# Performance work log

Measured on AMD Instinct MI355X. Metric: run time of the kernel, lower is better.

## Reference

```python
import jax, jax.numpy as jnp
import numpy as np
from jax import lax

NUM_TAGS = 64

def setup_inputs() -> dict:
    key = jax.random.key(0)
    ks = jax.random.split(key, 6)
    B, T, D, N = 64, 512, 1024, NUM_TAGS
    inputs = jax.random.normal(ks[0], (B, T, D), dtype=jnp.float32)
    mask = jnp.ones((B, T), dtype=jnp.int32)
    labels = jax.random.randint(ks[1], (B, T), 0, N)
    W = jax.random.normal(ks[2], (D, N), dtype=jnp.float32) / np.sqrt(D).astype(np.float32)
    b = jnp.zeros((N,), dtype=jnp.float32)
    transitions = jax.random.normal(ks[3], (N, N), dtype=jnp.float32) * 0.1
    start_transitions = jax.random.normal(ks[4], (N,), dtype=jnp.float32) * 0.1
    end_transitions = jax.random.normal(ks[5], (N,), dtype=jnp.float32) * 0.1
    return dict(inputs=inputs, mask=mask, labels=labels, W=W, b=b,
                transitions=transitions, start_transitions=start_transitions,
                end_transitions=end_transitions)


def _log_partition(logits, mask, trans, start, end):
    # forward algorithm (log-sum-exp recurrence). logits [B,T,N], mask bool [B,T]
    alpha = start[None, :] + logits[:, 0]                      # [B,N]
    emits = jnp.swapaxes(logits, 0, 1)[1:]                     # [T-1,B,N]
    ms = jnp.swapaxes(mask, 0, 1)[1:, :, None]                 # [T-1,B,1]
    def step(alpha, xs):
        emit, m = xs
        inner = alpha[:, :, None] + trans[None] + emit[:, None, :]  # [B,from,to]
        new = jax.nn.logsumexp(inner, axis=1)
        return jnp.where(m, new, alpha), None
    alpha, _ = lax.scan(step, alpha, (emits, ms))
    return jax.nn.logsumexp(alpha + end[None, :], axis=-1)     # [B]


def _joint_score(logits, tags, mask, trans, start, end):
    # score of the gold tag sequence (AllenNLP _joint_likelihood), vectorized
    maskf = mask.astype(logits.dtype)
    score = start[tags[:, 0]]
    score = score + jnp.sum(trans[tags[:, :-1], tags[:, 1:]] * maskf[:, 1:], axis=1)
    emit = jnp.take_along_axis(logits, tags[:, :, None], axis=2)[:, :, 0]   # [B,T]
    score = score + jnp.sum(emit * maskf, axis=1)
    last_idx = jnp.sum(mask.astype(jnp.int32), axis=1) - 1
    last_tags = jnp.take_along_axis(tags, last_idx[:, None], axis=1)[:, 0]
    return score + end[last_tags]


def _viterbi(logits, mask, trans, start, end):
    # batched Viterbi decode with backpointers; masked steps carry state through
    B, T, N = logits.shape
    alpha = start[None, :] + logits[:, 0]
    emits = jnp.swapaxes(logits, 0, 1)[1:]
    ms = jnp.swapaxes(mask, 0, 1)[1:, :, None]
    ident = jnp.broadcast_to(jnp.arange(N, dtype=jnp.int32)[None, :], (B, N))
    def step(alpha, xs):
        emit, m = xs
        sc = alpha[:, :, None] + trans[None] + emit[:, None, :]  # [B,from,to]
        best = jnp.max(sc, axis=1)
        bp = jnp.argmax(sc, axis=1).astype(jnp.int32)
        return jnp.where(m, best, alpha), jnp.where(m, bp, ident)
    alpha, bps = lax.scan(step, alpha, (emits, ms))
    last_tag = jnp.argmax(alpha + end[None, :], axis=-1).astype(jnp.int32)
    def back(tag, bp):
        prev = jnp.take_along_axis(bp, tag[:, None], axis=1)[:, 0]
        return prev, tag
    first, rest = lax.scan(back, last_tag, bps, reverse=True)
    tags = jnp.concatenate([first[None], rest], axis=0)          # [T,B]
    return jnp.swapaxes(tags, 0, 1) * mask.astype(jnp.int32)     # zero out padding


def reference(inputs, mask, labels, W, b, transitions, start_transitions, end_transitions):
    bool_mask = mask.astype(bool)
    logits = inputs @ W + b                                      # tag projection [B,T,N]
    scores = logits * mask[..., None].astype(logits.dtype)       # scores = inputs * mask
    tags = _viterbi(scores, bool_mask, transitions, start_transitions, end_transitions)
    log_z = _log_partition(scores, bool_mask, transitions, start_transitions, end_transitions)
    gold = _joint_score(scores, labels, bool_mask, transitions, start_transitions, end_transitions)
    loss = jnp.mean(log_z - gold)                                # mean negative log-likelihood
    return scores, tags, loss
```

## Files before the change

### kernel.cpp

```cpp
#include <hip/hip_runtime.h>
#include <cstdint>
#include <cstddef>

#define BB 64
#define TT 512
#define DD 1024
#define NTAG 64
#define CUT 255
#define SCORES_ELEMS (BB * TT * NTAG)
#define TAGS_OFF SCORES_ELEMS
#define LOSS_OFF (SCORES_ELEMS + BB * TT)

typedef __attribute__((ext_vector_type(8))) short short8;
typedef __attribute__((ext_vector_type(4))) float floatx4;
typedef __attribute__((ext_vector_type(16))) float f32x16;

__device__ __forceinline__ unsigned short f2bf_rne(float x) {
  const unsigned int u = __float_as_uint(x);
  const unsigned int r = u + 0x7FFFu + ((u >> 16) & 1u);
  return (unsigned short)(r >> 16);
}
__device__ __forceinline__ float bf2f(unsigned short h) {
  return __uint_as_float(((unsigned int)h) << 16);
}

__device__ __forceinline__ void block_sync_lds() {
  asm volatile("s_waitcnt lgkmcnt(0)\n\ts_barrier" ::: "memory");
}

__device__ __forceinline__ float quad_xor1(float v) {
  int x = __builtin_amdgcn_update_dpp(__float_as_int(v), __float_as_int(v), 0xB1, 0xf, 0xf, false);
  return __int_as_float(x);
}
__device__ __forceinline__ float quad_xor2(float v) {
  int x = __builtin_amdgcn_update_dpp(__float_as_int(v), __float_as_int(v), 0x4E, 0xf, 0xf, false);
  return __int_as_float(x);
}

__device__ __forceinline__ float dpp_red_max(float v) {
  int x;
  x = __builtin_amdgcn_update_dpp(__float_as_int(v), __float_as_int(v), 0x111, 0xf, 0xf, false);
  v = fmaxf(v, __int_as_float(x));
  x = __builtin_amdgcn_update_dpp(__float_as_int(v), __float_as_int(v), 0x112, 0xf, 0xf, false);
  v = fmaxf(v, __int_as_float(x));
  x = __builtin_amdgcn_update_dpp(__float_as_int(v), __float_as_int(v), 0x114, 0xf, 0xf, false);
  v = fmaxf(v, __int_as_float(x));
  x = __builtin_amdgcn_update_dpp(__float_as_int(v), __float_as_int(v), 0x118, 0xf, 0xf, false);
  v = fmaxf(v, __int_as_float(x));
  x = __builtin_amdgcn_update_dpp(__float_as_int(v), __float_as_int(v), 0x142, 0xa, 0xf, false);
  v = fmaxf(v, __int_as_float(x));
  x = __builtin_amdgcn_update_dpp(__float_as_int(v), __float_as_int(v), 0x143, 0xc, 0xf, false);
  v = fmaxf(v, __int_as_float(x));
  return __int_as_float(__builtin_amdgcn_readlane(__float_as_int(v), 63));
}

__device__ __forceinline__ float dpp_red_sum(float v) {
  int x;
  x = __builtin_amdgcn_update_dpp(__float_as_int(v), __float_as_int(v), 0x111, 0xf, 0xf, false);
  v = v + __int_as_float(x);
  x = __builtin_amdgcn_update_dpp(__float_as_int(v), __float_as_int(v), 0x112, 0xf, 0xf, false);
  v = v + __int_as_float(x);
  x = __builtin_amdgcn_update_dpp(__float_as_int(v), __float_as_int(v), 0x114, 0xf, 0xf, false);
  v = v + __int_as_float(x);
  x = __builtin_amdgcn_update_dpp(__float_as_int(v), __float_as_int(v), 0x118, 0xf, 0xf, false);
  v = v + __int_as_float(x);
  x = __builtin_amdgcn_update_dpp(__float_as_int(v), __float_as_int(v), 0x142, 0xa, 0xf, false);
  v = v + __int_as_float(x);
  x = __builtin_amdgcn_update_dpp(__float_as_int(v), __float_as_int(v), 0x143, 0xc, 0xf, false);
  v = v + __int_as_float(x);
  return __int_as_float(__builtin_amdgcn_readlane(__float_as_int(v), 63));
}

__global__ __launch_bounds__(256) void prep_w(
    const float* __restrict__ W, unsigned short* __restrict__ wf_hi,
    unsigned short* __restrict__ wf_lo) {
  const int f = blockIdx.x * 256 + threadIdx.x;
  const int kk = f >> 8;
  const int nt = (f >> 6) & 3;
  const int l = f & 63;
  const int n = nt * 16 + (l & 15);
  const int k0 = kk * 32 + ((l >> 4) << 3);
  short8 hv, lv;
#pragma unroll
  for (int j = 0; j < 8; ++j) {
    const float x = W[(size_t)(k0 + j) * NTAG + n];
    const unsigned short h = f2bf_rne(x);
    hv[j] = (short)h;
    lv[j] = (short)f2bf_rne(x - bf2f(h));
  }
  *reinterpret_cast<short8*>(wf_hi + (size_t)f * 8) = hv;
  *reinterpret_cast<short8*>(wf_lo + (size_t)f * 8) = lv;
}

__global__ __launch_bounds__(256) void gemm_scores(
    const float* __restrict__ X, const int* __restrict__ mask,
    const unsigned short* __restrict__ wf_hi,
    const unsigned short* __restrict__ wf_lo,
    const float* __restrict__ bias, float* __restrict__ scores) {
  __shared__ unsigned short xhi[64 * 72];
  __shared__ unsigned short xlo[64 * 72];
  const int tid = threadIdx.x;
  const int lane = tid & 63;
  const int wv = tid >> 6;
  const int row0 = blockIdx.x * 64;
  const int srow = tid >> 2;
  const int scg = tid & 3;
  const float* Xp = X + (size_t)(row0 + srow) * DD + scg * 16;

  floatx4 acc[4];
#pragma unroll
  for (int nt = 0; nt < 4; ++nt) acc[nt] = (floatx4)(0.f);

  float4 px[4];
#pragma unroll
  for (int p = 0; p < 4; ++p) px[p] = *reinterpret_cast<const float4*>(Xp + p * 4);

  const int arow = (wv << 4) + (lane & 15);
  const int aq = (lane >> 4) << 3;

  for (int c = 0; c < 16; ++c) {
    __syncthreads();
    short8 hb0, hb1, lb0, lb1;
#pragma unroll
    for (int p = 0; p < 4; ++p) {
      const float v[4] = {px[p].x, px[p].y, px[p].z, px[p].w};
#pragma unroll
      for (int e = 0; e < 4; ++e) {
        const unsigned short h = f2bf_rne(v[e]);
        const unsigned short lo2 = f2bf_rne(v[e] - bf2f(h));
        const int idx = p * 4 + e;
        if (idx < 8) { hb0[idx] = (short)h; lb0[idx] = (short)lo2; }
        else         { hb1[idx - 8] = (short)h; lb1[idx - 8] = (short)lo2; }
      }
    }
    {
      const int base = srow * 72 + scg * 16;
      *reinterpret_cast<short8*>(&xhi[base]) = hb0;
      *reinterpret_cast<short8*>(&xhi[base + 8]) = hb1;
      *reinterpret_cast<short8*>(&xlo[base]) = lb0;
      *reinterpret_cast<short8*>(&xlo[base + 8]) = lb1;
    }
    const int cn = (c < 15) ? (c + 1) : 0;
#pragma unroll
    for (int p = 0; p < 4; ++p)
      px[p] = *reinterpret_cast<const float4*>(Xp + cn * 64 + p * 4);
    __syncthreads();

#pragma unroll
    for (int sub = 0; sub < 2; ++sub) {
      const int kkAbs = c * 2 + sub;
      const short8 ah = *reinterpret_cast<const short8*>(&xhi[arow * 72 + sub * 32 + aq]);
      const short8 al = *reinterpret_cast<const short8*>(&xlo[arow * 72 + sub * 32 + aq]);
      const size_t fbase = (size_t)kkAbs * 4 * 64 * 8;
#pragma unroll
      for (int nt = 0; nt < 4; ++nt) {
        const size_t off = fbase + ((size_t)nt * 64 + lane) * 8;
        const short8 bh = *reinterpret_cast<const short8*>(wf_hi + off);
        const short8 bl = *reinterpret_cast<const short8*>(wf_lo + off);
        acc[nt] = __builtin_amdgcn_mfma_f32_16x16x32_bf16(ah, bh, acc[nt], 0, 0, 0);
        acc[nt] = __builtin_amdgcn_mfma_f32_16x16x32_bf16(ah, bl, acc[nt], 0, 0, 0);
        acc[nt] = __builtin_amdgcn_mfma_f32_16x16x32_bf16(al, bh, acc[nt], 0, 0, 0);
      }
    }
  }

  const int colb = lane & 15;
  const int quad = lane >> 4;
#pragma unroll
  for (int r = 0; r < 4; ++r) {
    const int row = row0 + (wv << 4) + quad * 4 + r;
    const float mf = (float)mask[row];
#pragma unroll
    for (int nt = 0; nt < 4; ++nt) {
      const int col = nt * 16 + colb;
      scores[(size_t)row * 64 + col] = (acc[nt][r] + bias[col]) * mf;
    }
  }
}

__global__ __launch_bounds__(256, 1) void crf_forward(
    const float* __restrict__ scores, const int* __restrict__ mask,
    const float* __restrict__ trans, const float* __restrict__ startv,
    const float* __restrict__ endv, float* __restrict__ ws_alpha,
    float* __restrict__ ws_beta, float* __restrict__ zAcut,
    float* __restrict__ bScut, float* __restrict__ bVcut,
    float* __restrict__ Ca, float* __restrict__ Cb) {
  __shared__ float zbuf[2][NTAG];
  __shared__ float part[4];
  const int tid = threadIdx.x;
  const int wv = tid >> 6;
  const int lane = tid & 63;
  const int q = lane & 3;
  const int jl = lane >> 2;
  const int j = wv * 16 + jl;
  const int role = blockIdx.x >> 6;
  const int b = blockIdx.x & 63;
  const float* sc = scores + (size_t)b * TT * NTAG;
  const int* maskb = mask + b * TT;

  if (role == 0) {
    f32x16 tc;
#pragma unroll
    for (int i2 = 0; i2 < 16; ++i2)
      tc[i2] = trans[(size_t)(16 * q + i2) * NTAG + j];

    float aj = startv[j] + sc[j];
    if (q == 0) zbuf[0][j] = aj;
    float* wsA = ws_alpha + (size_t)b * 256 * NTAG;

    float e0 = sc[1 * NTAG + j], e1 = sc[2 * NTAG + j];
    float e2 = sc[3 * NTAG + j], e3 = sc[4 * NTAG + j];
    int k0 = maskb[1], k1 = maskb[2], k2 = maskb[3], k3 = maskb[4];
    __syncthreads();

    int cur = 0;
    for (int t = 1; t <= CUT; ++t) {
      if (q == 0) wsA[(size_t)(t - 1) * NTAG + j] = aj;
      const float4 a0 = *reinterpret_cast<const float4*>(&zbuf[cur][q * 16 + 0]);
      const float4 a1 = *reinterpret_cast<const float4*>(&zbuf[cur][q * 16 + 4]);
      const float4 a2 = *reinterpret_cast<const float4*>(&zbuf[cur][q * 16 + 8]);
      const float4 a3 = *reinterpret_cast<const float4*>(&zbuf[cur][q * 16 + 12]);
      const float emit = e0;
      const int m = k0;
      const int tp = (t + 4 <= CUT) ? (t + 4) : CUT;
      e0 = e1; e1 = e2; e2 = e3;
      e3 = sc[(size_t)tp * NTAG + j];
      k0 = k1; k1 = k2; k2 = k3;
      k3 = maskb[tp];

      const float c0 = a0.x + tc[0],  c1 = a0.y + tc[1];
      const float c2 = a0.z + tc[2],  c3 = a0.w + tc[3];
      const float c4 = a1.x + tc[4],  c5 = a1.y + tc[5];
      const float c6 = a1.z + tc[6],  c7 = a1.w + tc[7];
      const float c8 = a2.x + tc[8],  c9 = a2.y + tc[9];
      const float cA = a2.z + tc[10], cB = a2.w + tc[11];
      const float cC = a3.x + tc[12], cD = a3.y + tc[13];
      const float cE = a3.z + tc[14], cF = a3.w + tc[15];
      const float h0 = fmaxf(fmaxf(c0, c1), fmaxf(c2, c3));
      const float h1 = fmaxf(fmaxf(c4, c5), fmaxf(c6, c7));
      const float h2 = fmaxf(fmaxf(c8, c9), fmaxf(cA, cB));
      const float h3 = fmaxf(fmaxf(cC, cD), fmaxf(cE, cF));
      float pm = fmaxf(fmaxf(h0, h1), fmaxf(h2, h3));
      pm = fmaxf(pm, quad_xor1(pm));
      pm = fmaxf(pm, quad_xor2(pm));

      aj = m ? (pm + emit) : aj;
      const int nxt = cur ^ 1;
      if (q == 0) zbuf[nxt][j] = aj;
      block_sync_lds();
      cur = nxt;
    }
    if (q == 0) wsA[(size_t)255 * NTAG + j] = aj;
  } else if (role == 1) {
    f32x16 ec;
#pragma unroll
    for (int i2 = 0; i2 < 16; ++i2)
      ec[i2] = expf(trans[(size_t)(16 * q + i2) * NTAG + j]);

    const float a0v = startv[j] + sc[j];
    const float wm = dpp_red_max(a0v);
    if (lane == 0) part[wv] = wm;
    __syncthreads();
    const float M0 = fmaxf(fmaxf(part[0], part[1]), fmaxf(part[2], part[3]));
    float zj = expf(a0v - M0);
    float C = M0;
    if (q == 0) zbuf[0][j] = zj;

    float e0 = sc[1 * NTAG + j], e1 = sc[2 * NTAG + j];
    float e2 = sc[3 * NTAG + j], e3 = sc[4 * NTAG + j];
    int k0 = maskb[1], k1 = maskb[2], k2 = maskb[3], k3 = maskb[4];
    float pe = expf(e0);
    __syncthreads();

    int cur = 0;
    for (int t = 1; t <= CUT; ++t) {
      const float4 z0 = *reinterpret_cast<const float4*>(&zbuf[cur][q * 16 + 0]);
      const float4 z1 = *reinterpret_cast<const float4*>(&zbuf[cur][q * 16 + 4]);
      const float4 z2 = *reinterpret_cast<const float4*>(&zbuf[cur][q * 16 + 8]);
      const float4 z3 = *reinterpret_cast<const float4*>(&zbuf[cur][q * 16 + 12]);
      const float pec = pe;
      const int m = k0;
      const int tp = (t + 4 <= CUT) ? (t + 4) : CUT;
      e0 = e1; e1 = e2; e2 = e3;
      e3 = sc[(size_t)tp * NTAG + j];
      k0 = k1; k1 = k2; k2 = k3;
      k3 = maskb[tp];
      pe = expf(e0);

      float s0 = z0.x * ec[0], s1 = z0.y * ec[1];
      float s2 = z0.z * ec[2], s3 = z0.w * ec[3];
      s0 = fmaf(z1.x, ec[4], s0);  s1 = fmaf(z1.y, ec[5], s1);
      s2 = fmaf(z1.z, ec[6], s2);  s3 = fmaf(z1.w, ec[7], s3);
      s0 = fmaf(z2.x, ec[8], s0);  s1 = fmaf(z2.y, ec[9], s1);
      s2 = fmaf(z2.z, ec[10], s2); s3 = fmaf(z2.w, ec[11], s3);
      s0 = fmaf(z3.x, ec[12], s0); s1 = fmaf(z3.y, ec[13], s1);
      s2 = fmaf(z3.z, ec[14], s2); s3 = fmaf(z3.w, ec[15], s3);
      float s = (s0 + s1) + (s2 + s3);
      s += quad_xor1(s);
      s += quad_xor2(s);

      zj = m ? (s * pec) : zj;

      if ((t & 7) == 0) {
        const float ws = dpp_red_sum(zj);
        if (lane == 0) part[wv] = ws;
        block_sync_lds();
        const float S4 = (part[0] + part[1]) + (part[2] + part[3]);
        const float r = __builtin_amdgcn_rcpf(S4);
        zj *= 4.0f * r;
        C += logf(S4) - 1.3862943611198906f;
      }

      const int nxt = cur ^ 1;
      if (q == 0) zbuf[nxt][j] = zj;
      block_sync_lds();
      cur = nxt;
    }
    if (q == 0) zAcut[b * NTAG + j] = zj;
    if (tid == 0) Ca[b] = C;
  } else if (role == 2) {
    f32x16 tc;
#pragma unroll
    for (int i2 = 0; i2 < 16; ++i2)
      tc[i2] = trans[(size_t)j * NTAG + 16 * q + i2];

    float bj = endv[j];
    float* wsB = ws_beta + (size_t)b * 256 * NTAG;
    if (q == 0) {
      wsB[(size_t)255 * NTAG + j] = bj;
      zbuf[0][j] = bj + sc[(size_t)511 * NTAG + j];
    }
    float e0 = sc[(size_t)510 * NTAG + j], e1 = sc[(size_t)509 * NTAG + j];
    float e2 = sc[(size_t)508 * NTAG + j], e3 = sc[(size_t)507 * NTAG + j];
    int k0 = maskb[511], k1 = maskb[510], k2 = maskb[509], k3 = maskb[508];
    __syncthreads();

    int cur = 0;
    for (int t = 511; t >= 257; --t) {
      const float4 a0 = *reinterpret_cast<const float4*>(&zbuf[cur][q * 16 + 0]);
      const float4 a1 = *reinterpret_cast<const float4*>(&zbuf[cur][q * 16 + 4]);
      const float4 a2 = *reinterpret_cast<const float4*>(&zbuf[cur][q * 16 + 8]);
      const float4 a3 = *reinterpret_cast<const float4*>(&zbuf[cur][q * 16 + 12]);
      const float emit = e0;
      const int m = k0;
      const int tpe = (t - 5 >= 0) ? (t - 5) : 0;
      const int tpk = (t - 4 >= 256) ? (t - 4) : 256;
      e0 = e1; e1 = e2; e2 = e3;
      e3 = sc[(size_t)tpe * NTAG + j];
      k0 = k1; k1 = k2; k2 = k3;
      k3 = maskb[tpk];

      const float c0 = a0.x + tc[0],  c1 = a0.y + tc[1];
      const float c2 = a0.z + tc[2],  c3 = a0.w + tc[3];
      const float c4 = a1.x + tc[4],  c5 = a1.y + tc[5];
      const float c6 = a1.z + tc[6],  c7 = a1.w + tc[7];
      const float c8 = a2.x + tc[8],  c9 = a2.y + tc[9];
      const float cA = a2.z + tc[10], cB = a2.w + tc[11];
      const float cC = a3.x + tc[12], cD = a3.y + tc[13];
      const float cE = a3.z + tc[14], cF = a3.w + tc[15];
      const float h0 = fmaxf(fmaxf(c0, c1), fmaxf(c2, c3));
      const float h1 = fmaxf(fmaxf(c4, c5), fmaxf(c6, c7));
      const float h2 = fmaxf(fmaxf(c8, c9), fmaxf(cA, cB));
      const float h3 = fmaxf(fmaxf(cC, cD), fmaxf(cE, cF));
      float pm = fmaxf(fmaxf(h0, h1), fmaxf(h2, h3));
      pm = fmaxf(pm, quad_xor1(pm));
      pm = fmaxf(pm, quad_xor2(pm));

      bj = m ? pm : bj;
      const int nxt = cur ^ 1;
      if (q == 0) {
        wsB[(size_t)(t - 1 - 256) * NTAG + j] = bj;
        zbuf[nxt][j] = bj + emit;
      }
      block_sync_lds();
      cur = nxt;
    }
    {
      const float4 a0 = *reinterpret_cast<const float4*>(&zbuf[cur][q * 16 + 0]);
      const float4 a1 = *reinterpret_cast<const float4*>(&zbuf[cur][q * 16 + 4]);
      const float4 a2 = *reinterpret_cast<const float4*>(&zbuf[cur][q * 16 + 8]);
      const float4 a3 = *reinterpret_cast<const float4*>(&zbuf[cur][q * 16 + 12]);
      const float c0 = a0.x + tc[0],  c1 = a0.y + tc[1];
      const float c2 = a0.z + tc[2],  c3 = a0.w + tc[3];
      const float c4 = a1.x + tc[4],  c5 = a1.y + tc[5];
      const float c6 = a1.z + tc[6],  c7 = a1.w + tc[7];
      const float c8 = a2.x + tc[8],  c9 = a2.y + tc[9];
      const float cA = a2.z + tc[10], cB = a2.w + tc[11];
      const float cC = a3.x + tc[12], cD = a3.y + tc[13];
      const float cE = a3.z + tc[14], cF = a3.w + tc[15];
      const float h0 = fmaxf(fmaxf(c0, c1), fmaxf(c2, c3));
      const float h1 = fmaxf(fmaxf(c4, c5), fmaxf(c6, c7));
      const float h2 = fmaxf(fmaxf(c8, c9), fmaxf(cA, cB));
      const float h3 = fmaxf(fmaxf(cC, cD), fmaxf(cE, cF));
      float pm = fmaxf(fmaxf(h0, h1), fmaxf(h2, h3));
      pm = fmaxf(pm, quad_xor1(pm));
      pm = fmaxf(pm, quad_xor2(pm));
      bj = k0 ? pm : bj;
      if (q == 0) bVcut[b * NTAG + j] = bj;
    }
  } else {
    f32x16 ec;
#pragma unroll
    for (int i2 = 0; i2 < 16; ++i2)
      ec[i2] = expf(trans[(size_t)j * NTAG + 16 * q + i2]);

    float bj = expf(endv[j]);
    float C = 0.f;
    if (q == 0) zbuf[0][j] = bj * expf(sc[(size_t)511 * NTAG + j]);
    float e0 = sc[(size_t)510 * NTAG + j], e1 = sc[(size_t)509 * NTAG + j];
    float e2 = sc[(size_t)508 * NTAG + j], e3 = sc[(size_t)507 * NTAG + j];
    int k0 = maskb[511], k1 = maskb[510], k2 = maskb[509], k3 = maskb[508];
    float pe = expf(e0);
    __syncthreads();

    int cur = 0;
    for (int t = 511; t >= 257; --t) {
      const float4 z0 = *reinterpret_cast<const float4*>(&zbuf[cur][q * 16 + 0]);
      const float4 z1 = *reinterpret_cast<const float4*>(&zbuf[cur][q * 16 + 4]);
      const float4 z2 = *reinterpret_cast<const float4*>(&zbuf[cur][q * 16 + 8]);
      const float4 z3 = *reinterpret_cast<const float4*>(&zbuf[cur][q * 16 + 12]);
      const float pec = pe;
      const int m = k0;
      const int tpe = (t - 5 >= 0) ? (t - 5) : 0;
      const int tpk = (t - 4 >= 256) ? (t - 4) : 256;
      e0 = e1; e1 = e2; e2 = e3;
      e3 = sc[(size_t)tpe * NTAG + j];
      k0 = k1; k1 = k2; k2 = k3;
      k3 = maskb[tpk];
      pe = expf(e0);

      float s0 = z0.x * ec[0], s1 = z0.y * ec[1];
      float s2 = z0.z * ec[2], s3 = z0.w * ec[3];
      s0 = fmaf(z1.x, ec[4], s0);  s1 = fmaf(z1.y, ec[5], s1);
      s2 = fmaf(z1.z, ec[6], s2);  s3 = fmaf(z1.w, ec[7], s3);
      s0 = fmaf(z2.x, ec[8], s0);  s1 = fmaf(z2.y, ec[9], s1);
      s2 = fmaf(z2.z, ec[10], s2); s3 = fmaf(z2.w, ec[11], s3);
      s0 = fmaf(z3.x, ec[12], s0); s1 = fmaf(z3.y, ec[13], s1);
      s2 = fmaf(z3.z, ec[14], s2); s3 = fmaf(z3.w, ec[15], s3);
      float s = (s0 + s1) + (s2 + s3);
      s += quad_xor1(s);
      s += quad_xor2(s);

      bj = m ? s : bj;

      if ((t & 7) == 0) {
        const float ws = dpp_red_sum(bj);
        if (lane == 0) part[wv] = ws;
        block_sync_lds();
        const float S4 = (part[0] + part[1]) + (part[2] + part[3]);
        const float r = __builtin_amdgcn_rcpf(S4);
        bj *= 4.0f * r;
        C += logf(S4) - 1.3862943611198906f;
      }

      const int nxt = cur ^ 1;
      if (q == 0) zbuf[nxt][j] = bj * pec;
      block_sync_lds();
      cur = nxt;
    }
    {
      const float4 z0 = *reinterpret_cast<const float4*>(&zbuf[cur][q * 16 + 0]);
      const float4 z1 = *reinterpret_cast<const float4*>(&zbuf[cur][q * 16 + 4]);
      const float4 z2 = *reinterpret_cast<const float4*>(&zbuf[cur][q * 16 + 8]);
      const float4 z3 = *reinterpret_cast<const float4*>(&zbuf[cur][q * 16 + 12]);
      float s0 = z0.x * ec[0], s1 = z0.y * ec[1];
      float s2 = z0.z * ec[2], s3 = z0.w * ec[3];
      s0 = fmaf(z1.x, ec[4], s0);  s1 = fmaf(z1.y, ec[5], s1);
      s2 = fmaf(z1.z, ec[6], s2);  s3 = fmaf(z1.w, ec[7], s3);
      s0 = fmaf(z2.x, ec[8], s0);  s1 = fmaf(z2.y, ec[9], s1);
      s2 = fmaf(z2.z, ec[10], s2); s3 = fmaf(z2.w, ec[11], s3);
      s0 = fmaf(z3.x, ec[12], s0); s1 = fmaf(z3.y, ec[13], s1);
      s2 = fmaf(z3.z, ec[14], s2); s3 = fmaf(z3.w, ec[15], s3);
      float s = (s0 + s1) + (s2 + s3);
      s += quad_xor1(s);
      s += quad_xor2(s);
      bj = k0 ? s : bj;
      if (q == 0) bScut[b * NTAG + j] = bj;
      if (tid == 0) Cb[b] = C;
    }
  }
}

__global__ __launch_bounds__(64, 1) void crf_combine(
    const float* __restrict__ scores, const int* __restrict__ mask,
    const int* __restrict__ labels, const float* __restrict__ trans,
    const float* __restrict__ startv, const float* __restrict__ endv,
    const float* __restrict__ ws_alpha, const float* __restrict__ bVcut,
    const float* __restrict__ zAcut, const float* __restrict__ bScut,
    const float* __restrict__ Ca, const float* __restrict__ Cb,
    int* __restrict__ ws_lasttag, float* __restrict__ ws_loss) {
  const int lane = threadIdx.x;
  const int b = blockIdx.x;
  const float* sc = scores + (size_t)b * TT * NTAG;
  const int* maskb = mask + b * TT;

  const float aV = ws_alpha[((size_t)b * 256 + 255) * NTAG + lane];
  const float fv = aV + bVcut[b * NTAG + lane];
  const float mx = dpp_red_max(fv);
  const int jstar = (int)__builtin_ctzll(__ballot(fv == mx));
  if (lane == 0) ws_lasttag[b] = jstar;

  const float S = dpp_red_sum(zAcut[b * NTAG + lane] * bScut[b * NTAG + lane]);
  const float log_z = logf(S) + Ca[b] + Cb[b];

  float g = 0.f, msumf = 0.f;
  for (int t = lane; t < TT; t += 64) {
    const int lab = labels[b * TT + t];
    const float mf = (float)maskb[t];
    msumf += mf;
    g += sc[(size_t)t * NTAG + lab] * mf;
    if (t >= 1) {
      const int labp = labels[b * TT + t - 1];
      g += trans[(size_t)labp * NTAG + lab] * mf;
    }
  }
  g = dpp_red_sum(g);
  const float msum = dpp_red_sum(msumf);
  const int last_idx = (int)msum - 1;
  g += startv[labels[b * TT]] + endv[labels[b * TT + last_idx]];
  if (lane == 0) ws_loss[b] = log_z - g;
}

__global__ __launch_bounds__(64, 1) void viterbi_bt(
    const float* __restrict__ ws_alpha, const float* __restrict__ ws_beta,
    const int* __restrict__ ws_lasttag, const int* __restrict__ mask,
    const float* __restrict__ scores, const float* __restrict__ trans,
    float* __restrict__ out_tags) {
  __shared__ float tP[NTAG * 65];
  __shared__ int mk[256];
  __shared__ unsigned char tagb[256];
  const int lane = threadIdx.x;
  const int role = blockIdx.x >> 6;
  const int b = blockIdx.x & 63;

#pragma unroll
  for (int i = 0; i < NTAG; ++i) tP[i * 65 + lane] = trans[(size_t)i * NTAG + lane];
  const int tbase = role * 256;
  for (int t = lane; t < 256; t += 64) mk[t] = mask[b * TT + tbase + t];
  __syncthreads();

  int jcur = ws_lasttag[b];

  if (role == 0) {
    const float* wsA = ws_alpha + (size_t)b * 256 * NTAG;
    if (lane == 0) tagb[255] = (unsigned char)jcur;

    float a0 = wsA[(size_t)254 * NTAG + lane];
    float a1 = wsA[(size_t)253 * NTAG + lane];
    float a2 = wsA[(size_t)252 * NTAG + lane];
    float a3 = wsA[(size_t)251 * NTAG + lane];

    for (int s = 254; s >= 0; --s) {
      const float ac = a0;
      a0 = a1; a1 = a2; a2 = a3;
      const int sp = (s >= 4) ? (s - 4) : 0;
      a3 = wsA[(size_t)sp * NTAG + lane];
      if (mk[s + 1]) {
        const float c = ac + tP[lane * 65 + jcur];
        const float cmx = dpp_red_max(c);
        jcur = (int)__builtin_ctzll(__ballot(c == cmx));
      }
      if (lane == 0) tagb[s] = (unsigned char)jcur;
    }
  } else {
    const float* wsB = ws_beta + (size_t)b * 256 * NTAG;
    const float* scb = scores + (size_t)b * TT * NTAG;
    float r0 = wsB[(size_t)0 * NTAG + lane], r1 = wsB[(size_t)1 * NTAG + lane];
    float r2 = wsB[(size_t)2 * NTAG + lane], r3 = wsB[(size_t)3 * NTAG + lane];
    float s0 = scb[(size_t)256 * NTAG + lane], s1 = scb[(size_t)257 * NTAG + lane];
    float s2 = scb[(size_t)258 * NTAG + lane], s3 = scb[(size_t)259 * NTAG + lane];

    for (int t = 256; t < TT; ++t) {
      const float bv = r0, sv = s0;
      const int tb = (t + 4 < TT) ? (t + 4) : (TT - 1);
      r0 = r1; r1 = r2; r2 = r3;
      r3 = wsB[(size_t)(tb - 256) * NTAG + lane];
      s0 = s1; s1 = s2; s2 = s3;
      s3 = scb[(size_t)tb * NTAG + lane];
      if (mk[t - 256]) {
        const float c = tP[jcur * 65 + lane] + sv + bv;
        const float cmx = dpp_red_max(c);
        jcur = (int)__builtin_ctzll(__ballot(c == cmx));
      }
      if (lane == 0) tagb[t - 256] = (unsigned char)jcur;
    }
  }
  __syncthreads();
  for (int t = lane; t < 256; t += 64)
    out_tags[b * TT + tbase + t] = (float)(mk[t] ? (int)tagb[t] : 0);
}

__global__ __launch_bounds__(64, 1) void loss_mean(const float* __restrict__ ws_loss,
                                                   float* __restrict__ out) {
  const float v = ws_loss[threadIdx.x];
  const float s = dpp_red_sum(v);
  if (threadIdx.x == 0) out[0] = s * (1.0f / 64.0f);
}

extern "C" void kernel_launch(void* const* d_in, const int* in_sizes, int n_in,
                              void* d_out, int out_size, void* d_ws, size_t ws_size,
                              hipStream_t stream) {
  const float* X = (const float*)d_in[0];
  const int* mask = (const int*)d_in[1];
  const int* labels = (const int*)d_in[2];
  const float* W = (const float*)d_in[3];
  const float* bias = (const float*)d_in[4];
  const float* trans = (const float*)d_in[5];
  const float* startv = (const float*)d_in[6];
  const float* endv = (const float*)d_in[7];

  float* out = (float*)d_out;
  float* scores = out;
  float* out_tags = out + TAGS_OFF;
  float* out_loss = out + LOSS_OFF;

  unsigned short* wf_hi = (unsigned short*)d_ws;
  unsigned short* wf_lo = wf_hi + 65536;
  float* ws_alpha = (float*)(wf_lo + 65536);
  float* ws_beta = ws_alpha + (size_t)BB * 256 * NTAG;
  float* zAcut = ws_beta + (size_t)BB * 256 * NTAG;
  float* bScut = zAcut + BB * NTAG;
  float* bVcut = bScut + BB * NTAG;
  float* Ca = bVcut + BB * NTAG;
  float* Cb = Ca + BB;
  int* ws_lasttag = (int*)(Cb + BB);
  float* ws_loss = (float*)(ws_lasttag + BB);

  prep_w<<<32, 256, 0, stream>>>(W, wf_hi, wf_lo);
  gemm_scores<<<512, 256, 0, stream>>>(X, mask, wf_hi, wf_lo, bias, scores);
  crf_forward<<<256, 256, 0, stream>>>(scores, mask, trans, startv, endv,
                                       ws_alpha, ws_beta, zAcut, bScut, bVcut,
                                       Ca, Cb);
  crf_combine<<<64, 64, 0, stream>>>(scores, mask, labels, trans, startv, endv,
                                     ws_alpha, bVcut, zAcut, bScut, Ca, Cb,
                                     ws_lasttag, ws_loss);
  viterbi_bt<<<128, 64, 0, stream>>>(ws_alpha, ws_beta, ws_lasttag, mask,
                                     scores, trans, out_tags);
  loss_mean<<<1, 64, 0, stream>>>(ws_loss, out_loss);
}
```

Baseline: 394.0 us.

## Split GEMM K dimension across waves with LDS reduction, shrink row tile

The scores GEMM now gives each block 16 rows instead of 64 and splits the K=1024 reduction across the four waves, 256 each. Each wave loads its X fragment straight from global into registers, so the LDS staging and per-chunk barriers are gone. A single LDS reduction at the end combines the partial sums, and the grid grows to 2048 blocks with a higher occupancy hint. This is meant to expose more parallelism and memory-level concurrency for this memory-bound GEMM, at the cost of an extra reduction step and each block rereading all of W.

```diff
diff --git a/kernel.cpp b/kernel.cpp
--- a/kernel.cpp
+++ b/kernel.cpp
@@ -92,88 +92,84 @@
   *reinterpret_cast<short8*>(wf_lo + (size_t)f * 8) = lv;
 }
 
-__global__ __launch_bounds__(256) void gemm_scores(
+__global__ __launch_bounds__(256, 6) void gemm_scores(
     const float* __restrict__ X, const int* __restrict__ mask,
     const unsigned short* __restrict__ wf_hi,
     const unsigned short* __restrict__ wf_lo,
     const float* __restrict__ bias, float* __restrict__ scores) {
-  __shared__ unsigned short xhi[64 * 72];
-  __shared__ unsigned short xlo[64 * 72];
+  __shared__ float red[3 * 64 * 17];
   const int tid = threadIdx.x;
   const int lane = tid & 63;
   const int wv = tid >> 6;
-  const int row0 = blockIdx.x * 64;
-  const int srow = tid >> 2;
-  const int scg = tid & 3;
-  const float* Xp = X + (size_t)(row0 + srow) * DD + scg * 16;
+  const int row0 = blockIdx.x * 16;
+  const int arow = row0 + (lane & 15);
+  const int aq = (lane >> 4) << 3;
+  const float* Ap = X + (size_t)arow * DD + wv * 256 + aq;
 
   floatx4 acc[4];
 #pragma unroll
   for (int nt = 0; nt < 4; ++nt) acc[nt] = (floatx4)(0.f);
 
-  float4 px[4];
-#pragma unroll
-  for (int p = 0; p < 4; ++p) px[p] = *reinterpret_cast<const float4*>(Xp + p * 4);
-
-  const int arow = (wv << 4) + (lane & 15);
-  const int aq = (lane >> 4) << 3;
-
-  for (int c = 0; c < 16; ++c) {
-    __syncthreads();
-    short8 hb0, hb1, lb0, lb1;
-#pragma unroll
-    for (int p = 0; p < 4; ++p) {
-      const float v[4] = {px[p].x, px[p].y, px[p].z, px[p].w};
-#pragma unroll
-      for (int e = 0; e < 4; ++e) {
+  float4 a0 = *reinterpret_cast<const float4*>(Ap);
+  float4 a1 = *reinterpret_cast<const float4*>(Ap + 4);
+
+#pragma unroll
+  for (int kk = 0; kk < 8; ++kk) {
+    short8 ah, al;
+    {
+      const float v[8] = {a0.x, a0.y, a0.z, a0.w, a1.x, a1.y, a1.z, a1.w};
+#pragma unroll
+      for (int e = 0; e < 8; ++e) {
         const unsigned short h = f2bf_rne(v[e]);
-        const unsigned short lo2 = f2bf_rne(v[e] - bf2f(h));
-        const int idx = p * 4 + e;
-        if (idx < 8) { hb0[idx] = (short)h; lb0[idx] = (short)lo2; }
-        else         { hb1[idx - 8] = (short)h; lb1[idx - 8] = (short)lo2; }
+        ah[e] = (short)h;
+        al[e] = (short)f2bf_rne(v[e] - bf2f(h));
       }
     }
-    {
-      const int base = srow * 72 + scg * 16;
-      *reinterpret_cast<short8*>(&xhi[base]) = hb0;
-      *reinterpret_cast<short8*>(&xhi[base + 8]) = hb1;
-      *reinterpret_cast<short8*>(&xlo[base]) = lb0;
-      *reinterpret_cast<short8*>(&xlo[base + 8]) = lb1;
-    }
-    const int cn = (c < 15) ? (c + 1) : 0;
-#pragma unroll
-    for (int p = 0; p < 4; ++p)
-      px[p] = *reinterpret_cast<const float4*>(Xp + cn * 64 + p * 4);
-    __syncthreads();
-
-#pragma unroll
-    for (int sub = 0; sub < 2; ++sub) {
-      const int kkAbs = c * 2 + sub;
-      const short8 ah = *reinterpret_cast<const short8*>(&xhi[arow * 72 + sub * 32 + aq]);
-      const short8 al = *reinterpret_cast<const short8*>(&xlo[arow * 72 + sub * 32 + aq]);
-      const size_t fbase = (size_t)kkAbs * 4 * 64 * 8;
+    if (kk < 7) {
+      a0 = *reinterpret_cast<const float4*>(Ap + (kk + 1) * 32);
+      a1 = *reinterpret_cast<const float4*>(Ap + (kk + 1) * 32 + 4);
+    }
+    const int kkAbs = wv * 8 + kk;
+    const size_t fbase = (size_t)kkAbs * 4 * 64 * 8;
+#pragma unroll
+    for (int nt = 0; nt < 4; ++nt) {
+      const size_t off = fbase + ((size_t)nt * 64 + lane) * 8;
+      const short8 bh = *reinterpret_cast<const short8*>(wf_hi + off);
+      const short8 bl = *reinterpret_cast<const short8*>(wf_lo + off);
+      acc[nt] = __builtin_amdgcn_mfma_f32_16x16x32_bf16(ah, bh, acc[nt], 0, 0, 0);
+      acc[nt] = __builtin_amdgcn_mfma_f32_16x16x32_bf16(ah, bl, acc[nt], 0, 0, 0);
+      acc[nt] = __builtin_amdgcn_mfma_f32_16x16x32_bf16(al, bh, acc[nt], 0, 0, 0);
+    }
+  }
+
+  if (wv > 0) {
+    float* dst = &red[((wv - 1) * 64 + lane) * 17];
+#pragma unroll
+    for (int nt = 0; nt < 4; ++nt)
+#pragma unroll
+      for (int r = 0; r < 4; ++r) dst[nt * 4 + r] = acc[nt][r];
+  }
+  __syncthreads();
+  if (wv == 0) {
+#pragma unroll
+    for (int w = 0; w < 3; ++w) {
+      const float* srcp = &red[(w * 64 + lane) * 17];
+#pragma unroll
+      for (int nt = 0; nt < 4; ++nt)
+#pragma unroll
+        for (int r = 0; r < 4; ++r) acc[nt][r] += srcp[nt * 4 + r];
+    }
+    const int colb = lane & 15;
+    const int quad = lane >> 4;
+#pragma unroll
+    for (int r = 0; r < 4; ++r) {
+      const int row = row0 + quad * 4 + r;
+      const float mf = (float)mask[row];
 #pragma unroll
       for (int nt = 0; nt < 4; ++nt) {
-        const size_t off = fbase + ((size_t)nt * 64 + lane) * 8;
-        const short8 bh = *reinterpret_cast<const short8*>(wf_hi + off);
-        const short8 bl = *reinterpret_cast<const short8*>(wf_lo + off);
-        acc[nt] = __builtin_amdgcn_mfma_f32_16x16x32_bf16(ah, bh, acc[nt], 0, 0, 0);
-        acc[nt] = __builtin_amdgcn_mfma_f32_16x16x32_bf16(ah, bl, acc[nt], 0, 0, 0);
-        acc[nt] = __builtin_amdgcn_mfma_f32_16x16x32_bf16(al, bh, acc[nt], 0, 0, 0);
+        const int col = nt * 16 + colb;
+        scores[(size_t)row * 64 + col] = (acc[nt][r] + bias[col]) * mf;
       }
-    }
-  }
-
-  const int colb = lane & 15;
-  const int quad = lane >> 4;
-#pragma unroll
-  for (int r = 0; r < 4; ++r) {
-    const int row = row0 + (wv << 4) + quad * 4 + r;
-    const float mf = (float)mask[row];
-#pragma unroll
-    for (int nt = 0; nt < 4; ++nt) {
-      const int col = nt * 16 + colb;
-      scores[(size_t)row * 64 + col] = (acc[nt][r] + bias[col]) * mf;
     }
   }
 }
@@ -627,7 +623,7 @@
   float* ws_loss = (float*)(ws_lasttag + BB);
 
   prep_w<<<32, 256, 0, stream>>>(W, wf_hi, wf_lo);
-  gemm_scores<<<512, 256, 0, stream>>>(X, mask, wf_hi, wf_lo, bias, scores);
+  gemm_scores<<<2048, 256, 0, stream>>>(X, mask, wf_hi, wf_lo, bias, scores);
   crf_forward<<<256, 256, 0, stream>>>(scores, mask, trans, startv, endv,
                                        ws_alpha, ws_beta, zAcut, bScut, bVcut,
                                        Ca, Cb);
```

After: 388.8 us. Within noise of the previous version (-1.3%).
